# Optimization experiments

Hardware: AMD Instinct MI355X
Metric: run time of the kernel (lower is better)

## Reference

```python
import jax, jax.numpy as jnp
import numpy as np

D = 2560
H = 64
HD = D // H  # 40
TE = 512
FF = 4 * D  # 10240
EPS = 1e-5


def _ln(x, eps=EPS):
    # fp32 layernorm, no affine
    x32 = x.astype(jnp.float32)
    mu = jnp.mean(x32, axis=-1, keepdims=True)
    var = jnp.var(x32, axis=-1, keepdims=True)
    return ((x32 - mu) * jax.lax.rsqrt(var + eps)).astype(x.dtype)


def _rope(x, cos, sin):
    # x: [B, H, S_img, HD]; cos/sin: [S_img, HD]
    half = x.shape[-1] // 2
    xr, xi = x[..., :half], x[..., half:]
    x_rot = jnp.concatenate([-xi, xr], axis=-1)
    c = cos[None, None]
    s = sin[None, None]
    return (x.astype(jnp.float32) * c + x_rot.astype(jnp.float32) * s).astype(x.dtype)


def setup_inputs() -> dict:
    key = jax.random.key(0)
    ks = jax.random.split(key, 20)
    f = jnp.float32
    inp = {
        "hidden_states": jax.random.normal(ks[0], (1, 1024, D), f),
        "encoder_hidden_states": jax.random.normal(ks[1], (1, 128, D), f),
        "time_embed": jax.random.normal(ks[2], (1, TE), f),
        "rope_cos": jax.random.uniform(ks[3], (1024, HD), f),
        "rope_sin": jax.random.uniform(ks[4], (1024, HD), f),
        # AdaLayerNormZero linear: time_embed_dim -> 12*D
        "ada_w": jax.random.normal(ks[5], (TE, 12 * D), f) * 0.02,
        "ada_b": jnp.zeros((12 * D,), f),
        # attention projections (stored [in, out])
        "wq": jax.random.normal(ks[6], (D, D), f) * 0.02,
        "bq": jnp.zeros((D,), f),
        "wk": jax.random.normal(ks[7], (D, D), f) * 0.02,
        "bk": jnp.zeros((D,), f),
        "wv": jax.random.normal(ks[8], (D, D), f) * 0.02,
        "bv": jnp.zeros((D,), f),
        "wo": jax.random.normal(ks[9], (D, D), f) * 0.02,
        "bo": jnp.zeros((D,), f),
        # feedforward (shared for img and context streams)
        "w1": jax.random.normal(ks[10], (D, FF), f) * 0.02,
        "b1": jnp.zeros((FF,), f),
        "w2": jax.random.normal(ks[11], (FF, D), f) * 0.02,
        "b2": jnp.zeros((D,), f),
    }
    return inp


def _block(hidden_states, encoder_hidden_states, time_embed, rope_cos, rope_sin,
           ada_w, ada_b, wq, bq, wk, bk, wv, bv, wo, bo, w1, b1, w2, b2):
    B, T, _ = encoder_hidden_states.shape

    # --- AdaLayerNormZero ---
    emb = time_embed @ ada_w + ada_b  # [B, 12*D]
    (shift_msa, c_shift_msa, scale_msa, c_scale_msa, gate_msa, c_gate_msa,
     shift_mlp, c_shift_mlp, scale_mlp, c_scale_mlp, gate_mlp, c_gate_mlp) = jnp.split(emb, 12, axis=1)
    u = lambda v: v[:, None, :]  # [B,1,D]

    norm_h = _ln(hidden_states) * (1 + u(scale_msa)) + u(shift_msa)
    norm_e = _ln(encoder_hidden_states) * (1 + u(c_scale_msa)) + u(c_shift_msa)

    # --- SelfAttention on concatenated [text, image] sequence ---
    x = jnp.concatenate([norm_e, norm_h], axis=1)  # [B,S,D]
    S = x.shape[1]
    def heads(y):
        return y.reshape(B, S, H, HD).transpose(0, 2, 1, 3)  # [B,H,S,HD]
    q = heads(x @ wq + bq)
    k = heads(x @ wk + bk)
    v = heads(x @ wv + bv)
    q = _ln(q)  # fp32 QK-norm over head_dim
    k = _ln(k)
    # partial RoPE on image tokens only
    q = q.at[:, :, T:, :].set(_rope(q[:, :, T:, :], rope_cos, rope_sin))
    k = k.at[:, :, T:, :].set(_rope(k[:, :, T:, :], rope_cos, rope_sin))

    scores = jnp.einsum('bhqd,bhkd->bhqk', q, k) / np.sqrt(HD).astype(np.float32)
    attn = jax.nn.softmax(scores, axis=-1)
    o = jnp.einsum('bhqk,bhkd->bhqd', attn, v)  # [B,H,S,HD]
    o = o.transpose(0, 2, 1, 3).reshape(B, S, D)
    o = o @ wo + bo
    attn_e, attn_h = o[:, :T], o[:, T:]

    # --- residual with attn gates ---
    hidden_states = hidden_states + attn_h * u(gate_msa)
    encoder_hidden_states = encoder_hidden_states + attn_e * u(c_gate_msa)

    # --- MLP with AdaLN modulation + gates ---
    nh = _ln(hidden_states) * (1 + u(scale_mlp)) + u(shift_mlp)
    ne = _ln(encoder_hidden_states) * (1 + u(c_scale_mlp)) + u(c_shift_mlp)
    ff = lambda y: jax.nn.gelu(y @ w1 + b1, approximate=True) @ w2 + b2
    hidden_states = hidden_states + ff(nh) * u(gate_mlp)
    encoder_hidden_states = encoder_hidden_states + ff(ne) * u(c_gate_mlp)
    return hidden_states, encoder_hidden_states


def reference(hidden_states, encoder_hidden_states, time_embed, rope_cos, rope_sin,
              ada_w, ada_b, wq, bq, wk, bk, wv, bv, wo, bo, w1, b1, w2, b2):
    return _block(hidden_states, encoder_hidden_states, time_embed, rope_cos, rope_sin,
                  ada_w, ada_b, wq, bq, wk, bk, wv, bv, wo, bo, w1, b1, w2, b2)
```

## Files before the change

kernel.cpp:

```cpp
#include <hip/hip_runtime.h>
#include <stdint.h>

#define D 2560
#define NH 64
#define HD 40
#define TE_ 512
#define FFD 10240
#define TENC 128
#define THID 1024
#define SEQ 1152

typedef __bf16 bf16_t;
typedef __bf16 bf16x8 __attribute__((ext_vector_type(8)));
typedef float  f32x4  __attribute__((ext_vector_type(4)));

__device__ __forceinline__ void gld_lds16(const void* g, void* l) {
  __builtin_amdgcn_global_load_lds((__attribute__((address_space(1))) void*)(g),
                                   (__attribute__((address_space(3))) void*)(l), 16, 0, 0);
}

__device__ __forceinline__ void wtrans_tile(const float* __restrict__ W, bf16_t* __restrict__ Wt,
                                            int K, int N, int bk, int bn, int tid,
                                            float* tile ) {
  #pragma unroll
  for (int i = 0; i < 4; ++i) {
    int c = i * 256 + tid;
    int r = c >> 4, q = c & 15;
    f32x4 v = *(const f32x4*)(W + (size_t)(bk * 64 + r) * N + bn * 64 + q * 4);
    tile[r * 65 + q * 4 + 0] = v[0]; tile[r * 65 + q * 4 + 1] = v[1];
    tile[r * 65 + q * 4 + 2] = v[2]; tile[r * 65 + q * 4 + 3] = v[3];
  }
  __syncthreads();
  #pragma unroll
  for (int i = 0; i < 2; ++i) {
    int c = i * 256 + tid;
    int n = c >> 3, kc = c & 7;
    bf16x8 o;
    #pragma unroll
    for (int j = 0; j < 8; ++j) o[j] = (bf16_t)tile[(kc * 8 + j) * 65 + n];
    *(bf16x8*)(Wt + (size_t)(bn * 64 + n) * K + bk * 64 + kc * 8) = o;
  }
}

__global__ __launch_bounds__(256) void prep1(
    const float* __restrict__ te, const float* __restrict__ aw, const float* __restrict__ ab,
    float* __restrict__ emb,
    const float* __restrict__ wq, const float* __restrict__ wk, const float* __restrict__ wv,
    bf16_t* __restrict__ wqkvT,
    const float* __restrict__ bq, const float* __restrict__ bk, const float* __restrict__ bv,
    float* __restrict__ bqkv, bf16_t* __restrict__ vt) {
  __shared__ float tile[64 * 65];
  const int b = blockIdx.x, t = threadIdx.x;
  if (b < 120) {
    int j = b * 256 + t;
    float acc = ab[j];
    #pragma unroll 8
    for (int k = 0; k < TE_; ++k) acc = fmaf(te[k], aw[(size_t)k * (12 * D) + j], acc);
    emb[j] = acc;
  } else if (b < 1720) {
    int l = b - 120;  wtrans_tile(wq, wqkvT,                     D, D, l % 40, l / 40, t, tile);
  } else if (b < 3320) {
    int l = b - 1720; wtrans_tile(wk, wqkvT + (size_t)D * D,     D, D, l % 40, l / 40, t, tile);
  } else if (b < 4920) {
    int l = b - 3320; wtrans_tile(wv, wqkvT + (size_t)2 * D * D, D, D, l % 40, l / 40, t, tile);
  } else if (b < 4950) {
    int i = (b - 4920) * 256 + t;
    bqkv[i] = i < D ? bq[i] : (i < 2 * D ? bk[i - D] : bv[i - 2 * D]);
  } else {
    int i = (b - 4950) * 256 + t;
    int h = i / 1152, g = i - h * 1152;
    bf16x8 z = {};
    if (g < 144) {
      #pragma unroll
      for (int j = 0; j < 8; ++j) z[j] = (bf16_t)1.f;
    }
    *(bf16x8*)(vt + ((size_t)h * 48 + 40) * SEQ + g * 8) = z;
  }
}

__global__ void ln_mod(const float* __restrict__ hid, const float* __restrict__ enc,
                       const float* __restrict__ emb, bf16_t* __restrict__ out,
                       int shift_h, int scale_h, int shift_e, int scale_e) {
  int row = blockIdx.x, tid = threadIdx.x;
  const float *src, *sc, *sh;
  if (row < TENC) { src = enc + (size_t)row * D;          sc = emb + scale_e * D; sh = emb + shift_e * D; }
  else            { src = hid + (size_t)(row - TENC) * D; sc = emb + scale_h * D; sh = emb + shift_h * D; }
  float v[10], s = 0.f, s2 = 0.f;
  #pragma unroll
  for (int i = 0; i < 10; ++i) { v[i] = src[tid + i * 256]; s += v[i]; s2 += v[i] * v[i]; }
  #pragma unroll
  for (int o = 32; o > 0; o >>= 1) { s += __shfl_down(s, o); s2 += __shfl_down(s2, o); }
  __shared__ float red[8];
  int wv = tid >> 6, ln = tid & 63;
  if (ln == 0) { red[wv] = s; red[4 + wv] = s2; }
  __syncthreads();
  s  = red[0] + red[1] + red[2] + red[3];
  s2 = red[4] + red[5] + red[6] + red[7];
  float mean = s * (1.f / D);
  float rstd = rsqrtf(s2 * (1.f / D) - mean * mean + 1e-5f);
  #pragma unroll
  for (int i = 0; i < 10; ++i) {
    int c = tid + i * 256;
    out[(size_t)row * D + c] = (bf16_t)((v[i] - mean) * rstd * (1.f + sc[c]) + sh[c]);
  }
}

template<int EPI>
__device__ __forceinline__ void gemm_body(
    bf16_t* As, bf16_t* Bs,
    const bf16_t* __restrict__ A, const bf16_t* __restrict__ Bt,
    const float* __restrict__ bias, int Kld, int ksteps, int N, int nM, int nMN,
    int nwg, int orig,
    bf16_t* __restrict__ outb, float* __restrict__ outp) {
  const int q8 = nwg >> 3, r8 = nwg & 7;
  const int xcd = orig & 7, pos = orig >> 3;
  const int wg = (xcd < r8 ? xcd * (q8 + 1) : r8 * (q8 + 1) + (xcd - r8) * q8) + pos;
  const int part = wg / nMN, rest = wg - part * nMN;
  const int bm = rest % nM, bn = rest / nM;
  const int m0 = bm * 128, n0 = bn * 128;
  const int kbase = part * ksteps;
  const int tid = threadIdx.x, wv = tid >> 6, ln = tid & 63;
  const int wr = wv >> 1, wc = wv & 1, lr = ln & 15, lg = ln >> 4;

  f32x4 acc[4][4];
  const f32x4 zero = {0.f, 0.f, 0.f, 0.f};
  #pragma unroll
  for (int m = 0; m < 4; ++m)
    #pragma unroll
    for (int n = 0; n < 4; ++n) acc[m][n] = zero;

  for (int t = 0; t < ksteps; ++t) {
    const int k0 = (kbase + t) << 6;
    __syncthreads();
    #pragma unroll
    for (int i = 0; i < 4; ++i) {
      int g = wv * 4 + i;
      int s = g * 64 + ln;
      int r = s >> 3, ks = s & 7;
      gld_lds16(A + (size_t)(m0 + r) * Kld + k0 + ((ks ^ (r & 7)) << 3), &As[g * 512]);
    }
    #pragma unroll
    for (int i = 0; i < 4; ++i) {
      int g = wv * 4 + i;
      int s = g * 64 + ln;
      int r = s >> 3, ks = s & 7;
      gld_lds16(Bt + (size_t)(n0 + r) * Kld + k0 + ((ks ^ (r & 7)) << 3), &Bs[g * 512]);
    }
    __syncthreads();
    #pragma unroll
    for (int ks2 = 0; ks2 < 2; ++ks2) {
      int ko = ks2 * 4 + lg;
      bf16x8 af[4], bfr[4];
      #pragma unroll
      for (int m = 0; m < 4; ++m) {
        int r = wr * 64 + m * 16 + lr;
        af[m] = *(const bf16x8*)&As[r * 64 + ((ko ^ (r & 7)) << 3)];
      }
      #pragma unroll
      for (int n = 0; n < 4; ++n) {
        int c = wc * 64 + n * 16 + lr;
        bfr[n] = *(const bf16x8*)&Bs[c * 64 + ((ko ^ (c & 7)) << 3)];
      }
      #pragma unroll
      for (int m = 0; m < 4; ++m)
        #pragma unroll
        for (int n = 0; n < 4; ++n)
          acc[m][n] = __builtin_amdgcn_mfma_f32_16x16x32_bf16(af[m], bfr[n], acc[m][n], 0, 0, 0);
    }
  }

  #pragma unroll
  for (int m = 0; m < 4; ++m) {
    int row = m0 + wr * 64 + m * 16 + (lg << 2);
    #pragma unroll
    for (int n = 0; n < 4; ++n) {
      int col = n0 + wc * 64 + n * 16 + lr;
      float bv = (EPI == 4) ? 0.f : bias[col];
      #pragma unroll
      for (int r = 0; r < 4; ++r) {
        float val = acc[m][n][r] + bv;
        int rr = row + r;
        if (EPI == 1) {
          float z = 0.7978845608028654f * (val + 0.044715f * val * val * val);
          float t2 = 1.f - 2.f / (__expf(2.f * z) + 1.f);
          outb[(size_t)rr * N + col] = (bf16_t)(0.5f * val * (1.f + t2));
        } else {
          outp[(size_t)part * SEQ * N + (size_t)rr * N + col] = val;
        }
      }
    }
  }
}

template<int EPI>
__global__ __launch_bounds__(256, 4) void gemm4(
    const bf16_t* __restrict__ A, const bf16_t* __restrict__ Bt,
    const float* __restrict__ bias, int Kld, int ksteps, int N, int nM, int nMN,
    bf16_t* __restrict__ outb, float* __restrict__ outp) {
  __shared__ bf16_t As[128 * 64];
  __shared__ bf16_t Bs[128 * 64];
  gemm_body<EPI>(As, Bs, A, Bt, bias, Kld, ksteps, N, nM, nMN, gridDim.x, blockIdx.x,
                 outb, outp);
}

__global__ __launch_bounds__(256, 4) void qkv_g(
    const bf16_t* __restrict__ A, const bf16_t* __restrict__ wqkvT,
    float* __restrict__ qparts,
    const float* __restrict__ wo, bf16_t* __restrict__ woT) {
  __shared__ char smem[32768] __attribute__((aligned(16)));
  const int b = blockIdx.x;
  if (b < 1080) {
    gemm_body<4>((bf16_t*)smem, (bf16_t*)(smem + 16384), A, wqkvT, nullptr,
                 D, 20, 3 * D, 9, 540, 1080, b, nullptr, qparts);
  } else {
    int l = b - 1080;
    wtrans_tile(wo, woT, D, D, l % 40, l / 40, threadIdx.x, (float*)smem);
  }
}

__global__ __launch_bounds__(256, 4) void oproj_plus(
    const bf16_t* __restrict__ A, const bf16_t* __restrict__ woT,
    float* __restrict__ oparts,
    const float* __restrict__ w2, bf16_t* __restrict__ w2T) {
  __shared__ char smem[32768] __attribute__((aligned(16)));
  const int b = blockIdx.x;
  if (b < 360) {
    gemm_body<4>((bf16_t*)smem, (bf16_t*)(smem + 16384), A, woT, nullptr,
                 D, 20, D, 9, 180, 360, b, nullptr, oparts);
  } else {
    int l = b - 360;
    wtrans_tile(w2, w2T, FFD, D, l % 160, l / 160, threadIdx.x, (float*)smem);
  }
}

__global__ __launch_bounds__(256) void qkv_red(
    const float* __restrict__ parts, const float* __restrict__ bqkv,
    const float* __restrict__ rc, const float* __restrict__ rs,
    bf16_t* __restrict__ qb, bf16_t* __restrict__ kb, bf16_t* __restrict__ vt) {
  const int r = blockIdx.x, t = threadIdx.x;
  const int h = t >> 2, sub = t & 3;
  __shared__ float cs_s[HD], sn_s[HD];
  const bool rope = (r >= TENC);
  if (rope && t < 2 * HD) {
    if (t < HD) cs_s[t] = rc[(size_t)(r - TENC) * HD + t];
    else        sn_s[t - HD] = rs[(size_t)(r - TENC) * HD + (t - HD)];
  }
  const float* p0 = parts + (size_t)r * (3 * D);
  const float* p1 = p0 + (size_t)SEQ * (3 * D);
  const int cq = h * HD + sub * 10;
  float q[10], k[10], v[10];
  #pragma unroll
  for (int j = 0; j < 10; ++j) {
    q[j] = p0[cq + j] + p1[cq + j] + bqkv[cq + j];
    k[j] = p0[D + cq + j] + p1[D + cq + j] + bqkv[D + cq + j];
    v[j] = p0[2 * D + cq + j] + p1[2 * D + cq + j] + bqkv[2 * D + cq + j];
  }
  __syncthreads();
  float qs = 0.f, qs2 = 0.f, ks = 0.f, ks2 = 0.f;
  #pragma unroll
  for (int j = 0; j < 10; ++j) { qs += q[j]; qs2 += q[j] * q[j]; ks += k[j]; ks2 += k[j] * k[j]; }
  qs += __shfl_xor(qs, 1); qs += __shfl_xor(qs, 2);
  qs2 += __shfl_xor(qs2, 1); qs2 += __shfl_xor(qs2, 2);
  ks += __shfl_xor(ks, 1); ks += __shfl_xor(ks, 2);
  ks2 += __shfl_xor(ks2, 1); ks2 += __shfl_xor(ks2, 2);
  float qm = qs * (1.f / HD), km = ks * (1.f / HD);
  float qr = rsqrtf(qs2 * (1.f / HD) - qm * qm + 1e-5f);
  float kr = rsqrtf(ks2 * (1.f / HD) - km * km + 1e-5f);
  #pragma unroll
  for (int j = 0; j < 10; ++j) { q[j] = (q[j] - qm) * qr; k[j] = (k[j] - km) * kr; }
  if (rope) {
    float pq[10], pk[10];
    #pragma unroll
    for (int j = 0; j < 10; ++j) { pq[j] = __shfl_xor(q[j], 2); pk[j] = __shfl_xor(k[j], 2); }
    #pragma unroll
    for (int j = 0; j < 10; ++j) {
      int d = sub * 10 + j;
      float c = cs_s[d], s = sn_s[d];
      if (d < 20) { q[j] = q[j] * c - pq[j] * s; k[j] = k[j] * c - pk[j] * s; }
      else        { q[j] = q[j] * c + pq[j] * s; k[j] = k[j] * c + pk[j] * s; }
    }
  }
  bf16_t* qd = qb + ((size_t)h * SEQ + r) * 64;
  bf16_t* kd = kb + ((size_t)h * SEQ + r) * 64;
  const float qscale = 0.15811388300841897f;
  #pragma unroll
  for (int j = 0; j < 10; ++j) {
    int d = sub * 10 + j;
    qd[d] = (bf16_t)(q[j] * qscale);
    kd[d] = (bf16_t)k[j];
  }
  #pragma unroll
  for (int j = 0; j < 6; ++j) {
    int d = 40 + sub * 6 + j;
    qd[d] = (bf16_t)0.f; kd[d] = (bf16_t)0.f;
  }
  #pragma unroll
  for (int j = 0; j < 10; ++j) {
    int d = sub * 10 + j;
    vt[((size_t)h * 48 + d) * SEQ + r] = (bf16_t)v[j];
  }
}

template<int P>
__global__ void redk(const float* __restrict__ parts, const float* __restrict__ bias,
                     const float* __restrict__ emb, int gate_h, int gate_e,
                     const float* __restrict__ res_h, const float* __restrict__ res_e,
                     float* __restrict__ out_h, float* __restrict__ out_e) {
  int idx = blockIdx.x * 256 + threadIdx.x;
  int row = idx / (D / 4), col = (idx - row * (D / 4)) * 4;
  f32x4 s = *(const f32x4*)(bias + col);
  #pragma unroll
  for (int p = 0; p < P; ++p)
    s += *(const f32x4*)(parts + (size_t)p * SEQ * D + (size_t)row * D + col);
  const float* res; float* out; int g;
  int r2;
  if (row < TENC) { res = res_e; out = out_e; g = gate_e; r2 = row; }
  else            { res = res_h; out = out_h; g = gate_h; r2 = row - TENC; }
  f32x4 g4 = *(const f32x4*)(emb + (size_t)g * D + col);
  f32x4 rr4 = *(const f32x4*)(res + (size_t)r2 * D + col);
  f32x4 o;
  #pragma unroll
  for (int j = 0; j < 4; ++j) o[j] = rr4[j] + s[j] * g4[j];
  *(f32x4*)(out + (size_t)r2 * D + col) = o;
}

template<int P>
__global__ __launch_bounds__(256) void redk_ln(
    const float* __restrict__ parts, const float* __restrict__ bias,
    const float* __restrict__ emb, int gate_h, int gate_e,
    int shift_h, int scale_h, int shift_e, int scale_e,
    const float* __restrict__ res_h, const float* __restrict__ res_e,
    float* __restrict__ out_h, float* __restrict__ out_e, bf16_t* __restrict__ xout) {
  int row = blockIdx.x, tid = threadIdx.x;
  const float* res; float* out; int g, sh, sc; int r2;
  if (row < TENC) { res = res_e; out = out_e; g = gate_e; sh = shift_e; sc = scale_e; r2 = row; }
  else            { res = res_h; out = out_h; g = gate_h; sh = shift_h; sc = scale_h; r2 = row - TENC; }
  float v[10], s = 0.f, s2 = 0.f;
  #pragma unroll
  for (int i = 0; i < 10; ++i) {
    int c = tid + i * 256;
    float val = bias[c];
    #pragma unroll
    for (int p = 0; p < P; ++p) val += parts[(size_t)p * SEQ * D + (size_t)row * D + c];
    val = res[(size_t)r2 * D + c] + val * emb[(size_t)g * D + c];
    out[(size_t)r2 * D + c] = val;
    v[i] = val; s += val; s2 += val * val;
  }
  #pragma unroll
  for (int o = 32; o > 0; o >>= 1) { s += __shfl_down(s, o); s2 += __shfl_down(s2, o); }
  __shared__ float red[8];
  int wvv = tid >> 6, lnn = tid & 63;
  if (lnn == 0) { red[wvv] = s; red[4 + wvv] = s2; }
  __syncthreads();
  s  = red[0] + red[1] + red[2] + red[3];
  s2 = red[4] + red[5] + red[6] + red[7];
  float mean = s * (1.f / D);
  float rstd = rsqrtf(s2 * (1.f / D) - mean * mean + 1e-5f);
  #pragma unroll
  for (int i = 0; i < 10; ++i) {
    int c = tid + i * 256;
    xout[(size_t)row * D + c] =
        (bf16_t)((v[i] - mean) * rstd * (1.f + emb[(size_t)sc * D + c]) + emb[(size_t)sh * D + c]);
  }
}

__global__ __launch_bounds__(256) void attn_plus(
    const bf16_t* __restrict__ qb, const bf16_t* __restrict__ kb,
    const bf16_t* __restrict__ vt, bf16_t* __restrict__ obf,
    const float* __restrict__ w1, bf16_t* __restrict__ w1T) {
  __shared__ char smem[30720] __attribute__((aligned(16)));
  const int b = blockIdx.x;
  if (b >= 576) {
    int l = b - 576;
    wtrans_tile(w1, w1T, D, FFD, l % 40, l / 40, threadIdx.x, (float*)smem);
    return;
  }
  bf16_t* Ks = (bf16_t*)smem;
  bf16_t* Vs = (bf16_t*)(smem + 8192);
  bf16_t* Ps = (bf16_t*)(smem + 14336);
  const int h = b & 63;
  const int qblk = b >> 6;
  const int tid = threadIdx.x, wv = tid >> 6, ln = tid & 63;
  const int qbase = qblk * 128 + wv * 32;
  const int lr = ln & 15, lg = ln >> 4;

  bf16x8 af[2][2];
  #pragma unroll
  for (int qf = 0; qf < 2; ++qf) {
    const bf16_t* qp = qb + ((size_t)h * SEQ + qbase + qf * 16 + lr) * 64 + lg * 8;
    af[qf][0] = *(const bf16x8*)(qp);
    af[qf][1] = *(const bf16x8*)(qp + 32);
  }
  const f32x4 zero = {0.f, 0.f, 0.f, 0.f};
  f32x4 acc[2][3];
  #pragma unroll
  for (int qf = 0; qf < 2; ++qf) { acc[qf][0] = zero; acc[qf][1] = zero; acc[qf][2] = zero; }

  const bf16_t* kbh = kb + (size_t)h * SEQ * 64;
  const bf16_t* vth = vt + (size_t)h * 48 * SEQ;

  for (int kv0 = 0; kv0 < SEQ; kv0 += 64) {
    __syncthreads();
    #pragma unroll
    for (int i = 0; i < 2; ++i) {
      int g = wv * 2 + i;
      int slot = g * 64 + ln;
      int kr = slot >> 3, so = slot & 7;
      gld_lds16(kbh + (size_t)(kv0 + kr) * 64 + ((so ^ (kr & 7)) << 3), &Ks[g * 512]);
    }
    #pragma unroll
    for (int i = 0; i < 2; ++i) {
      int g = wv + 4 * i;
      if (g < 6) {
        int slot = g * 64 + ln;
        int dr = slot >> 3, so = slot & 7;
        gld_lds16(vth + (size_t)dr * SEQ + kv0 + ((so ^ (dr & 7)) << 3), &Vs[g * 512]);
      }
    }
    __syncthreads();
    #pragma unroll
    for (int nt = 0; nt < 4; ++nt) {
      int kvr = nt * 16 + lr;
      bf16x8 bk0 = *(const bf16x8*)&Ks[kvr * 64 + ((lg ^ (kvr & 7)) << 3)];
      bf16x8 bk1 = *(const bf16x8*)&Ks[kvr * 64 + (((4 + lg) ^ (kvr & 7)) << 3)];
      #pragma unroll
      for (int qf = 0; qf < 2; ++qf) {
        f32x4 s = zero;
        s = __builtin_amdgcn_mfma_f32_16x16x32_bf16(af[qf][0], bk0, s, 0, 0, 0);
        s = __builtin_amdgcn_mfma_f32_16x16x32_bf16(af[qf][1], bk1, s, 0, 0, 0);
        #pragma unroll
        for (int r = 0; r < 4; ++r) {
          float p = exp2f(fmaf(s[r], 1.44269504f, -9.377517766f));
          int q = lg * 4 + r;
          int kv = nt * 16 + lr;
          Ps[(wv * 2 + qf) * 1024 + q * 64 + ((((kv >> 3) ^ (q & 7)) << 3) | (kv & 7))] = (bf16_t)p;
        }
      }
    }
    bf16x8 pa[2][2];
    #pragma unroll
    for (int qf = 0; qf < 2; ++qf)
      #pragma unroll
      for (int kk = 0; kk < 2; ++kk)
        pa[qf][kk] = *(const bf16x8*)&Ps[(wv * 2 + qf) * 1024 + lr * 64 + (((kk * 4 + lg) ^ (lr & 7)) << 3)];
    #pragma unroll
    for (int dt = 0; dt < 3; ++dt) {
      int dr = dt * 16 + lr;
      #pragma unroll
      for (int kk = 0; kk < 2; ++kk) {
        bf16x8 bv = *(const bf16x8*)&Vs[dr * 64 + (((kk * 4 + lg) ^ (dr & 7)) << 3)];
        acc[0][dt] = __builtin_amdgcn_mfma_f32_16x16x32_bf16(pa[0][kk], bv, acc[0][dt], 0, 0, 0);
        acc[1][dt] = __builtin_amdgcn_mfma_f32_16x16x32_bf16(pa[1][kk], bv, acc[1][dt], 0, 0, 0);
      }
    }
  }
  #pragma unroll
  for (int qf = 0; qf < 2; ++qf) {
    float linv[4];
    #pragma unroll
    for (int r = 0; r < 4; ++r)
      linv[r] = 1.f / __shfl(acc[qf][2][r], (ln & 48) | 8);
    #pragma unroll
    for (int dt = 0; dt < 3; ++dt) {
      int d = dt * 16 + lr;
      if (d < HD) {
        #pragma unroll
        for (int r = 0; r < 4; ++r) {
          int q = qbase + qf * 16 + lg * 4 + r;
          obf[(size_t)q * D + h * HD + d] = (bf16_t)(acc[qf][dt][r] * linv[r]);
        }
      }
    }
  }
}

extern "C" void kernel_launch(void* const* d_in, const int* in_sizes, int n_in,
                              void* d_out, int out_size, void* d_ws, size_t ws_size,
                              hipStream_t stream) {
  const float* hid = (const float*)d_in[0];
  const float* enc = (const float*)d_in[1];
  const float* tem = (const float*)d_in[2];
  const float* rc  = (const float*)d_in[3];
  const float* rs  = (const float*)d_in[4];
  const float* aw  = (const float*)d_in[5];
  const float* ab  = (const float*)d_in[6];
  const float* wq  = (const float*)d_in[7];
  const float* bq  = (const float*)d_in[8];
  const float* wk  = (const float*)d_in[9];
  const float* bk  = (const float*)d_in[10];
  const float* wvv = (const float*)d_in[11];
  const float* bv  = (const float*)d_in[12];
  const float* wo  = (const float*)d_in[13];
  const float* bo  = (const float*)d_in[14];
  const float* w1  = (const float*)d_in[15];
  const float* b1  = (const float*)d_in[16];
  const float* w2  = (const float*)d_in[17];
  const float* b2  = (const float*)d_in[18];
  float* out_hid = (float*)d_out;
  float* out_enc = out_hid + (size_t)THID * D;

  char* ws = (char*)d_ws;
  size_t off = 0;
  auto alloc = [&](size_t b) { char* p = ws + off; off += (b + 255) & ~(size_t)255; return p; };
  float*  emb  = (float*) alloc((size_t)12 * D * 4);
  bf16_t* xln  = (bf16_t*)alloc((size_t)SEQ * D * 2);
  bf16_t* aff  = (bf16_t*)alloc((size_t)SEQ * FFD * 2);
  bf16_t* vt   = (bf16_t*)alloc((size_t)NH * 48 * SEQ * 2);
  bf16_t* qbb  = (bf16_t*)alloc((size_t)NH * SEQ * 64 * 2);
  bf16_t* kbb  = (bf16_t*)alloc((size_t)NH * SEQ * 64 * 2);
  bf16_t* wqkvT= (bf16_t*)alloc((size_t)3 * D * D * 2);
  bf16_t* woT  = (bf16_t*)alloc((size_t)D * D * 2);
  bf16_t* w1T  = (bf16_t*)alloc((size_t)FFD * D * 2);
  bf16_t* w2T  = (bf16_t*)alloc((size_t)D * FFD * 2);
  float*  bqkv = (float*) alloc((size_t)3 * D * 4);
  bf16_t* obf = xln;
  float*  h1  = (float*)qbb;
  float*  e1  = h1 + (size_t)THID * D;
  float*  qparts = (float*)w1T;
  float*  oparts = (float*)wqkvT;
  float*  fparts = (float*)wqkvT;

  prep1<<<dim3(5238), dim3(256), 0, stream>>>(tem, aw, ab, emb, wq, wk, wvv,
      wqkvT, bq, bk, bv, bqkv, vt);
  ln_mod<<<dim3(SEQ), dim3(256), 0, stream>>>(hid, enc, emb, xln, 0, 2, 1, 3);
  qkv_g<<<dim3(2680), dim3(256), 0, stream>>>(xln, wqkvT, qparts, wo, woT);
  qkv_red<<<dim3(SEQ), dim3(256), 0, stream>>>(qparts, bqkv, rc, rs, qbb, kbb, vt);
  attn_plus<<<dim3(6976), dim3(256), 0, stream>>>(qbb, kbb, vt, obf, w1, w1T);
  oproj_plus<<<dim3(6760), dim3(256), 0, stream>>>(obf, woT, oparts, w2, w2T);
  redk_ln<2><<<dim3(SEQ), dim3(256), 0, stream>>>(oparts, bo, emb, 4, 5, 6, 8, 7, 9,
      hid, enc, h1, e1, xln);
  gemm4<1><<<dim3(720), dim3(256), 0, stream>>>(xln, w1T, b1, D, 40, FFD, 9, 720,
      aff, nullptr);
  gemm4<4><<<dim3(720), dim3(256), 0, stream>>>(aff, w2T, nullptr, FFD, 40, D, 9, 180,
      nullptr, fparts);
  redk<4><<<dim3(2880), dim3(256), 0, stream>>>(fparts, b2, emb, 10, 11, h1, e1, out_hid, out_enc);
}
```

Before: 442.2 us.

## Split-K the AdaLN GEMV, widen attention query tiles, double split-K for FF2

Three independent changes. First, the AdaLN embedding GEMV now splits K across four wavefronts per block and reduces the partial sums in LDS, using four independent accumulators. This is meant to raise parallelism and memory-level parallelism over the old one-thread-per-output serial loop. Second, each attention wave now covers 48 queries instead of 32, so each K/V tile is reused across more query rows, at the cost of more registers and LDS. Third, the second FFN GEMM splits K into eight chunks instead of four, doubling its grid, with the reduction kernel reading eight partials; this adds partial-buffer traffic.

```diff
diff --git a/kernel.cpp b/kernel.cpp
--- a/kernel.cpp
+++ b/kernel.cpp
@@ -42,32 +42,44 @@
   }
 }
 
-__global__ __launch_bounds__(256) void prep1(
-    const float* __restrict__ te, const float* __restrict__ aw, const float* __restrict__ ab,
-    float* __restrict__ emb,
+__global__ __launch_bounds__(256) void ada_plus(
+    const float* __restrict__ te, const float* __restrict__ aw,
+    const float* __restrict__ ab, float* __restrict__ emb,
     const float* __restrict__ wq, const float* __restrict__ wk, const float* __restrict__ wv,
     bf16_t* __restrict__ wqkvT,
     const float* __restrict__ bq, const float* __restrict__ bk, const float* __restrict__ bv,
     float* __restrict__ bqkv, bf16_t* __restrict__ vt) {
   __shared__ float tile[64 * 65];
   const int b = blockIdx.x, t = threadIdx.x;
-  if (b < 120) {
-    int j = b * 256 + t;
-    float acc = ab[j];
+  if (b < 480) {
+    float* red = tile;
+    const int j = b * 64 + (t & 63);
+    const int kc = t >> 6;
+    const float* awp = aw + (size_t)(kc * 128) * (12 * D) + j;
+    const float* tep = te + kc * 128;
+    float a0 = 0.f, a1 = 0.f, a2 = 0.f, a3 = 0.f;
     #pragma unroll 8
-    for (int k = 0; k < TE_; ++k) acc = fmaf(te[k], aw[(size_t)k * (12 * D) + j], acc);
-    emb[j] = acc;
-  } else if (b < 1720) {
-    int l = b - 120;  wtrans_tile(wq, wqkvT,                     D, D, l % 40, l / 40, t, tile);
-  } else if (b < 3320) {
-    int l = b - 1720; wtrans_tile(wk, wqkvT + (size_t)D * D,     D, D, l % 40, l / 40, t, tile);
-  } else if (b < 4920) {
-    int l = b - 3320; wtrans_tile(wv, wqkvT + (size_t)2 * D * D, D, D, l % 40, l / 40, t, tile);
-  } else if (b < 4950) {
-    int i = (b - 4920) * 256 + t;
+    for (int k = 0; k < 128; k += 4) {
+      a0 = fmaf(tep[k],     awp[(size_t)k * (12 * D)],       a0);
+      a1 = fmaf(tep[k + 1], awp[(size_t)(k + 1) * (12 * D)], a1);
+      a2 = fmaf(tep[k + 2], awp[(size_t)(k + 2) * (12 * D)], a2);
+      a3 = fmaf(tep[k + 3], awp[(size_t)(k + 3) * (12 * D)], a3);
+    }
+    red[kc * 64 + (t & 63)] = (a0 + a1) + (a2 + a3);
+    __syncthreads();
+    if (t < 64)
+      emb[j] = ab[j] + red[t] + red[64 + t] + red[128 + t] + red[192 + t];
+  } else if (b < 2080) {
+    int l = b - 480;  wtrans_tile(wq, wqkvT,                     D, D, l % 40, l / 40, t, tile);
+  } else if (b < 3680) {
+    int l = b - 2080; wtrans_tile(wk, wqkvT + (size_t)D * D,     D, D, l % 40, l / 40, t, tile);
+  } else if (b < 5280) {
+    int l = b - 3680; wtrans_tile(wv, wqkvT + (size_t)2 * D * D, D, D, l % 40, l / 40, t, tile);
+  } else if (b < 5310) {
+    int i = (b - 5280) * 256 + t;
     bqkv[i] = i < D ? bq[i] : (i < 2 * D ? bk[i - D] : bv[i - 2 * D]);
   } else {
-    int i = (b - 4950) * 256 + t;
+    int i = (b - 5310) * 256 + t;
     int h = i / 1152, g = i - h * 1152;
     bf16x8 z = {};
     if (g < 144) {
@@ -368,10 +380,10 @@
     const bf16_t* __restrict__ qb, const bf16_t* __restrict__ kb,
     const bf16_t* __restrict__ vt, bf16_t* __restrict__ obf,
     const float* __restrict__ w1, bf16_t* __restrict__ w1T) {
-  __shared__ char smem[30720] __attribute__((aligned(16)));
+  __shared__ char smem[38912] __attribute__((aligned(16)));
   const int b = blockIdx.x;
-  if (b >= 576) {
-    int l = b - 576;
+  if (b >= 384) {
+    int l = b - 384;
     wtrans_tile(w1, w1T, D, FFD, l % 40, l / 40, threadIdx.x, (float*)smem);
     return;
   }
@@ -381,20 +393,20 @@
   const int h = b & 63;
   const int qblk = b >> 6;
   const int tid = threadIdx.x, wv = tid >> 6, ln = tid & 63;
-  const int qbase = qblk * 128 + wv * 32;
+  const int qbase = qblk * 192 + wv * 48;
   const int lr = ln & 15, lg = ln >> 4;
 
-  bf16x8 af[2][2];
-  #pragma unroll
-  for (int qf = 0; qf < 2; ++qf) {
+  bf16x8 af[3][2];
+  #pragma unroll
+  for (int qf = 0; qf < 3; ++qf) {
     const bf16_t* qp = qb + ((size_t)h * SEQ + qbase + qf * 16 + lr) * 64 + lg * 8;
     af[qf][0] = *(const bf16x8*)(qp);
     af[qf][1] = *(const bf16x8*)(qp + 32);
   }
   const f32x4 zero = {0.f, 0.f, 0.f, 0.f};
-  f32x4 acc[2][3];
-  #pragma unroll
-  for (int qf = 0; qf < 2; ++qf) { acc[qf][0] = zero; acc[qf][1] = zero; acc[qf][2] = zero; }
+  f32x4 acc[3][3];
+  #pragma unroll
+  for (int qf = 0; qf < 3; ++qf) { acc[qf][0] = zero; acc[qf][1] = zero; acc[qf][2] = zero; }
 
   const bf16_t* kbh = kb + (size_t)h * SEQ * 64;
   const bf16_t* vth = vt + (size_t)h * 48 * SEQ;
@@ -424,7 +436,7 @@
       bf16x8 bk0 = *(const bf16x8*)&Ks[kvr * 64 + ((lg ^ (kvr & 7)) << 3)];
       bf16x8 bk1 = *(const bf16x8*)&Ks[kvr * 64 + (((4 + lg) ^ (kvr & 7)) << 3)];
       #pragma unroll
-      for (int qf = 0; qf < 2; ++qf) {
+      for (int qf = 0; qf < 3; ++qf) {
         f32x4 s = zero;
         s = __builtin_amdgcn_mfma_f32_16x16x32_bf16(af[qf][0], bk0, s, 0, 0, 0);
         s = __builtin_amdgcn_mfma_f32_16x16x32_bf16(af[qf][1], bk1, s, 0, 0, 0);
@@ -433,16 +445,16 @@
           float p = exp2f(fmaf(s[r], 1.44269504f, -9.377517766f));
           int q = lg * 4 + r;
           int kv = nt * 16 + lr;
-          Ps[(wv * 2 + qf) * 1024 + q * 64 + ((((kv >> 3) ^ (q & 7)) << 3) | (kv & 7))] = (bf16_t)p;
+          Ps[(wv * 3 + qf) * 1024 + q * 64 + ((((kv >> 3) ^ (q & 7)) << 3) | (kv & 7))] = (bf16_t)p;
         }
       }
     }
-    bf16x8 pa[2][2];
-    #pragma unroll
-    for (int qf = 0; qf < 2; ++qf)
+    bf16x8 pa[3][2];
+    #pragma unroll
+    for (int qf = 0; qf < 3; ++qf)
       #pragma unroll
       for (int kk = 0; kk < 2; ++kk)
-        pa[qf][kk] = *(const bf16x8*)&Ps[(wv * 2 + qf) * 1024 + lr * 64 + (((kk * 4 + lg) ^ (lr & 7)) << 3)];
+        pa[qf][kk] = *(const bf16x8*)&Ps[(wv * 3 + qf) * 1024 + lr * 64 + (((kk * 4 + lg) ^ (lr & 7)) << 3)];
     #pragma unroll
     for (int dt = 0; dt < 3; ++dt) {
       int dr = dt * 16 + lr;
@@ -451,11 +463,12 @@
         bf16x8 bv = *(const bf16x8*)&Vs[dr * 64 + (((kk * 4 + lg) ^ (dr & 7)) << 3)];
         acc[0][dt] = __builtin_amdgcn_mfma_f32_16x16x32_bf16(pa[0][kk], bv, acc[0][dt], 0, 0, 0);
         acc[1][dt] = __builtin_amdgcn_mfma_f32_16x16x32_bf16(pa[1][kk], bv, acc[1][dt], 0, 0, 0);
-      }
-    }
-  }
-  #pragma unroll
-  for (int qf = 0; qf < 2; ++qf) {
+        acc[2][dt] = __builtin_amdgcn_mfma_f32_16x16x32_bf16(pa[2][kk], bv, acc[2][dt], 0, 0, 0);
+      }
+    }
+  }
+  #pragma unroll
+  for (int qf = 0; qf < 3; ++qf) {
     float linv[4];
     #pragma unroll
     for (int r = 0; r < 4; ++r)
@@ -520,18 +533,18 @@
   float*  oparts = (float*)wqkvT;
   float*  fparts = (float*)wqkvT;
 
-  prep1<<<dim3(5238), dim3(256), 0, stream>>>(tem, aw, ab, emb, wq, wk, wvv,
-      wqkvT, bq, bk, bv, bqkv, vt);
+  ada_plus<<<dim3(5598), dim3(256), 0, stream>>>(tem, aw, ab, emb,
+      wq, wk, wvv, wqkvT, bq, bk, bv, bqkv, vt);
   ln_mod<<<dim3(SEQ), dim3(256), 0, stream>>>(hid, enc, emb, xln, 0, 2, 1, 3);
   qkv_g<<<dim3(2680), dim3(256), 0, stream>>>(xln, wqkvT, qparts, wo, woT);
   qkv_red<<<dim3(SEQ), dim3(256), 0, stream>>>(qparts, bqkv, rc, rs, qbb, kbb, vt);
-  attn_plus<<<dim3(6976), dim3(256), 0, stream>>>(qbb, kbb, vt, obf, w1, w1T);
+  attn_plus<<<dim3(6784), dim3(256), 0, stream>>>(qbb, kbb, vt, obf, w1, w1T);
   oproj_plus<<<dim3(6760), dim3(256), 0, stream>>>(obf, woT, oparts, w2, w2T);
   redk_ln<2><<<dim3(SEQ), dim3(256), 0, stream>>>(oparts, bo, emb, 4, 5, 6, 8, 7, 9,
       hid, enc, h1, e1, xln);
   gemm4<1><<<dim3(720), dim3(256), 0, stream>>>(xln, w1T, b1, D, 40, FFD, 9, 720,
       aff, nullptr);
-  gemm4<4><<<dim3(720), dim3(256), 0, stream>>>(aff, w2T, nullptr, FFD, 40, D, 9, 180,
+  gemm4<4><<<dim3(1440), dim3(256), 0, stream>>>(aff, w2T, nullptr, FFD, 20, D, 9, 180,
       nullptr, fparts);
-  redk<4><<<dim3(2880), dim3(256), 0, stream>>>(fparts, b2, emb, 10, 11, h1, e1, out_hid, out_enc);
-}
+  redk<8><<<dim3(2880), dim3(256), 0, stream>>>(fparts, b2, emb, 10, 11, h1, e1, out_hid, out_enc);
+}
```

After: 435.0 us. About the same (-1.6%).
